# Performance work log

Hardware: AMD Instinct MI355X
Metric: run time of the kernel (lower is better)

## Reference

```python
import jax, jax.numpy as jnp
import numpy as np

N_NODES = 50000
N_EDGES = 1600000
IN_FEATS = 256
OUT_FEATS = 64


def setup_inputs() -> dict:
    key = jax.random.key(0)
    k1, k2, k3, k4, k5, k6 = jax.random.split(key, 6)
    feature = jax.random.normal(k1, (N_NODES, IN_FEATS), dtype=jnp.float32)
    src = jax.random.randint(k2, (N_EDGES,), 0, N_NODES, dtype=jnp.int32)
    dst = jax.random.randint(k3, (N_EDGES,), 0, N_NODES, dtype=jnp.int32)
    # parameters (xavier-ish scaling)
    W = jax.random.normal(k4, (OUT_FEATS, IN_FEATS), dtype=jnp.float32) * np.sqrt(2.0 / (IN_FEATS + OUT_FEATS))
    att_w = jax.random.normal(k5, (1, 2 * OUT_FEATS), dtype=jnp.float32) * np.sqrt(2.0 / (2 * OUT_FEATS + 1))
    bias = jax.random.normal(k6, (1, OUT_FEATS), dtype=jnp.float32) * np.sqrt(2.0 / (1 + OUT_FEATS))
    return {"feature": feature, "W": W, "att_w": att_w, "bias": bias, "src": src, "dst": dst}


def reference(feature, W, att_w, bias, src, dst):
    # Wh = linear(feature)   [N, out]
    Wh = feature @ W.T
    # concat([Wh_src, Wh_dst]) @ att_w.T  ==  Wh_src@a_src + Wh_dst@a_dst
    a_src = att_w[0, :OUT_FEATS]
    a_dst = att_w[0, OUT_FEATS:]
    el = Wh @ a_src  # [N]
    er = Wh @ a_dst  # [N]
    e = el[src] + er[dst]  # [E]
    e = jax.nn.leaky_relu(e, negative_slope=0.2)
    # segment softmax over incoming edges of each dst node
    e_max = jax.ops.segment_max(e, dst, num_segments=N_NODES)  # -inf for empty
    e_max = jnp.where(jnp.isfinite(e_max), e_max, 0.0)
    e_exp = jnp.exp(e - e_max[dst])
    denom = jax.ops.segment_sum(e_exp, dst, num_segments=N_NODES)
    alpha = e_exp / jnp.where(denom[dst] > 0, denom[dst], 1.0)  # [E]
    # scatter-weighted sum of source features
    h_new = jax.ops.segment_sum(alpha[:, None] * Wh[src], dst, num_segments=N_NODES)
    # residual + bias + activation
    h_new = h_new + Wh
    h_new = jax.nn.elu(h_new + bias)
    return h_new
```

## Files before the change

kernel.cpp:

```cpp
#include <hip/hip_runtime.h>
#include <hip/hip_bf16.h>
#include <math.h>

#define N_NODES 50000
#define N_EDGES 1600000
#define IN_F 256
#define OUT_F 64

#define NBUCKETS 196
#define CAP 10240
#define GEMM_BLOCKS 782
#define BK_BLOCKS 391
#define EPB 4096

typedef short short8 __attribute__((ext_vector_type(8)));
typedef float f32x4 __attribute__((ext_vector_type(4)));

__device__ __forceinline__ unsigned short f2bf(float f) {
    union { __hip_bfloat16 h; unsigned short u; } v;
    v.h = __float2bfloat16(f);
    return v.u;
}
__device__ __forceinline__ float bf2f(unsigned u) {
    return __uint_as_float(u << 16);
}

__global__ __launch_bounds__(256) void k_prep(const float* __restrict__ W,
                                              unsigned short* __restrict__ wfrag,
                                              int* __restrict__ cnt) {
    const int tid = threadIdx.x;
    if (blockIdx.x == 0 && tid < NBUCKETS) cnt[tid] = 0;
    int c = blockIdx.x * 256 + tid;
    int ct = c >> 9, kt = (c >> 6) & 7, cl = c & 63;
    int col = ct * 16 + (cl & 15);
    int kb = kt * 32 + 8 * (cl >> 4);
    const float* p = W + col * 256 + kb;
    float4 x = *(const float4*)p;
    float4 y = *(const float4*)(p + 4);
    short8 v;
    v[0] = f2bf(x.x); v[1] = f2bf(x.y); v[2] = f2bf(x.z); v[3] = f2bf(x.w);
    v[4] = f2bf(y.x); v[5] = f2bf(y.y); v[6] = f2bf(y.z); v[7] = f2bf(y.w);
    *(short8*)(wfrag + c * 8) = v;
}

__global__ __launch_bounds__(256) void k_main(const float* __restrict__ feat,
                                              const unsigned short* __restrict__ wfrag,
                                              const float* __restrict__ att_w,
                                              unsigned short* __restrict__ whb,
                                              float* __restrict__ el,
                                              float* __restrict__ er,
                                              const int* __restrict__ src,
                                              const int* __restrict__ dst,
                                              int* __restrict__ cnt,
                                              unsigned* __restrict__ pairs) {
    const int tid = threadIdx.x;

    if (blockIdx.x >= GEMM_BLOCKS) {
        __shared__ int lhist[NBUCKETS];
        __shared__ int lcur[NBUCKETS];
        const int beg = (blockIdx.x - GEMM_BLOCKS) * EPB;
        int end = beg + EPB; if (end > N_EDGES) end = N_EDGES;
        if (tid < NBUCKETS) lhist[tid] = 0;
        __syncthreads();
        for (int i = beg + tid; i < end; i += 256)
            atomicAdd(&lhist[dst[i] >> 8], 1);
        __syncthreads();
        if (tid < NBUCKETS) {
            int c = lhist[tid];
            lcur[tid] = c ? (tid * CAP + atomicAdd(&cnt[tid], c)) : 0;
        }
        __syncthreads();
        for (int i = beg + tid; i < end; i += 256) {
            int d = dst[i];
            int pos = atomicAdd(&lcur[d >> 8], 1);
            pairs[pos] = (unsigned)src[i] | ((unsigned)(d & 255) << 16);
        }
        return;
    }

    const int l = tid & 63, w = tid >> 6;
    const int l15 = l & 15, lg = l >> 4;
    const int wbase = blockIdx.x * 64 + w * 16;
    int ar = wbase + l15; if (ar > N_NODES - 1) ar = N_NODES - 1;
    const float* fbase = feat + (size_t)ar * IN_F + 8 * lg;
    const unsigned short* wfl = wfrag + l * 8;

    f32x4 acc[4];
    #pragma unroll
    for (int ct = 0; ct < 4; ++ct) acc[ct] = (f32x4){0.f, 0.f, 0.f, 0.f};

    float4 fa = *(const float4*)(fbase);
    float4 fb = *(const float4*)(fbase + 4);
    #pragma unroll
    for (int kt = 0; kt < 8; ++kt) {
        float4 na, nb;
        if (kt < 7) {
            na = *(const float4*)(fbase + (kt + 1) * 32);
            nb = *(const float4*)(fbase + (kt + 1) * 32 + 4);
        }
        short8 bf0 = *(const short8*)(wfl + (0 * 8 + kt) * 512);
        short8 bf1 = *(const short8*)(wfl + (1 * 8 + kt) * 512);
        short8 bf2 = *(const short8*)(wfl + (2 * 8 + kt) * 512);
        short8 bf3 = *(const short8*)(wfl + (3 * 8 + kt) * 512);
        short8 af;
        af[0] = f2bf(fa.x); af[1] = f2bf(fa.y); af[2] = f2bf(fa.z); af[3] = f2bf(fa.w);
        af[4] = f2bf(fb.x); af[5] = f2bf(fb.y); af[6] = f2bf(fb.z); af[7] = f2bf(fb.w);
        acc[0] = __builtin_amdgcn_mfma_f32_16x16x32_bf16(af, bf0, acc[0], 0, 0, 0);
        acc[1] = __builtin_amdgcn_mfma_f32_16x16x32_bf16(af, bf1, acc[1], 0, 0, 0);
        acc[2] = __builtin_amdgcn_mfma_f32_16x16x32_bf16(af, bf2, acc[2], 0, 0, 0);
        acc[3] = __builtin_amdgcn_mfma_f32_16x16x32_bf16(af, bf3, acc[3], 0, 0, 0);
        fa = na; fb = nb;
    }

    float asrc[4], adst[4];
    #pragma unroll
    for (int ct = 0; ct < 4; ++ct) {
        asrc[ct] = att_w[ct * 16 + l15];
        adst[ct] = att_w[64 + ct * 16 + l15];
    }
    #pragma unroll
    for (int j = 0; j < 4; ++j) {
        int row = wbase + lg * 4 + j;
        float vs = 0.f, vd = 0.f;
        #pragma unroll
        for (int ct = 0; ct < 4; ++ct) {
            float v = acc[ct][j];
            vs += v * asrc[ct];
            vd += v * adst[ct];
            if (row < N_NODES) whb[(size_t)row * OUT_F + ct * 16 + l15] = f2bf(v);
        }
        vs += __shfl_xor(vs, 1); vd += __shfl_xor(vd, 1);
        vs += __shfl_xor(vs, 2); vd += __shfl_xor(vd, 2);
        vs += __shfl_xor(vs, 4); vd += __shfl_xor(vd, 4);
        vs += __shfl_xor(vs, 8); vd += __shfl_xor(vd, 8);
        if (l15 == 0 && row < N_NODES) { el[row] = vs; er[row] = vd; }
    }
}

__global__ __launch_bounds__(1024) void k_build(const int* __restrict__ cnt,
                                                const unsigned* __restrict__ pairs,
                                                const float* __restrict__ el,
                                                const float* __restrict__ er,
                                                int* __restrict__ offs,
                                                int* __restrict__ oend,
                                                unsigned* __restrict__ csr) {
    __shared__ int lcnt[256], ssc[256], lcur[256];
    __shared__ float ler[256];
    const int b = blockIdx.x;
    const int t = threadIdx.x;
    const int ebeg = b * CAP;
    const int nE = cnt[b];

    if (t < 256) {
        lcnt[t] = 0;
        int node = b * 256 + t;
        ler[t] = (node < N_NODES) ? er[node] : 0.f;
    }
    __syncthreads();
    for (int i = t; i < nE; i += 1024)
        atomicAdd(&lcnt[(pairs[ebeg + i] >> 16) & 255], 1);
    __syncthreads();
    if (t < 256) ssc[t] = (lcnt[t] + 3) & ~3;
    __syncthreads();
    for (int d = 1; d < 256; d <<= 1) {
        int v = 0;
        if (t < 256 && t >= d) v = ssc[t - d];
        __syncthreads();
        if (t < 256) ssc[t] += v;
        __syncthreads();
    }
    if (t < 256) {
        int pc = (lcnt[t] + 3) & ~3;
        int base = ssc[t] - pc;
        lcur[t] = base;
        int node = b * 256 + t;
        if (node < N_NODES) { offs[node] = ebeg + base; oend[node] = ebeg + base + pc; }
        for (int k = lcnt[t]; k < pc; ++k) csr[ebeg + base + k] = 0;
    }
    __syncthreads();
    for (int i = t; i < nE; i += 1024) {
        unsigned v = pairs[ebeg + i];
        int n8 = (v >> 16) & 255;
        int s = v & 0xFFFFu;
        float e = el[s] + ler[n8];
        e = (e > 0.f) ? e : 0.2f * e;
        float p = __expf(e);
        int pos = atomicAdd(&lcur[n8], 1);
        csr[ebeg + pos] = (unsigned)s | ((unsigned)f2bf(p) << 16);
    }
}

__global__ __launch_bounds__(256) void k_aggr(const int* __restrict__ offs,
                                              const int* __restrict__ oend,
                                              const unsigned* __restrict__ csr,
                                              const unsigned short* __restrict__ whb,
                                              const float* __restrict__ bias,
                                              float* __restrict__ out) {
    const int wid = __builtin_amdgcn_readfirstlane(threadIdx.x >> 6);
    const int node = blockIdx.x * 4 + wid;
    const int lane = threadIdx.x & 63;
    const int fg = lane & 15, es = lane >> 4;
    const int beg = offs[node], end = oend[node];

    float acc0 = 0.f, acc1 = 0.f, acc2 = 0.f, acc3 = 0.f, den = 0.f;
    #pragma unroll 2
    for (int j = beg; j < end; j += 4) {
        unsigned e = csr[j + es];
        float p = __uint_as_float(e & 0xFFFF0000u);
        const unsigned short* wp = whb + (size_t)(e & 0xFFFFu) * OUT_F + fg * 4;
        ushort4 wv = *(const ushort4*)wp;
        den += p;
        acc0 = fmaf(p, bf2f((unsigned)wv.x), acc0);
        acc1 = fmaf(p, bf2f((unsigned)wv.y), acc1);
        acc2 = fmaf(p, bf2f((unsigned)wv.z), acc2);
        acc3 = fmaf(p, bf2f((unsigned)wv.w), acc3);
    }
    acc0 += __shfl_xor(acc0, 16); acc0 += __shfl_xor(acc0, 32);
    acc1 += __shfl_xor(acc1, 16); acc1 += __shfl_xor(acc1, 32);
    acc2 += __shfl_xor(acc2, 16); acc2 += __shfl_xor(acc2, 32);
    acc3 += __shfl_xor(acc3, 16); acc3 += __shfl_xor(acc3, 32);
    den  += __shfl_xor(den, 16);  den  += __shfl_xor(den, 32);

    if (es == 0) {
        float inv = (end > beg) ? 1.f / den : 0.f;
        ushort4 wn = *(const ushort4*)(whb + (size_t)node * OUT_F + fg * 4);
        float4 b4 = *(const float4*)(bias + fg * 4);
        float h0 = acc0 * inv + bf2f((unsigned)wn.x) + b4.x;
        float h1 = acc1 * inv + bf2f((unsigned)wn.y) + b4.y;
        float h2 = acc2 * inv + bf2f((unsigned)wn.z) + b4.z;
        float h3 = acc3 * inv + bf2f((unsigned)wn.w) + b4.w;
        h0 = (h0 > 0.f) ? h0 : __expf(h0) - 1.f;
        h1 = (h1 > 0.f) ? h1 : __expf(h1) - 1.f;
        h2 = (h2 > 0.f) ? h2 : __expf(h2) - 1.f;
        h3 = (h3 > 0.f) ? h3 : __expf(h3) - 1.f;
        *(float4*)(out + (size_t)node * OUT_F + fg * 4) = make_float4(h0, h1, h2, h3);
    }
}

extern "C" void kernel_launch(void* const* d_in, const int* in_sizes, int n_in,
                              void* d_out, int out_size, void* d_ws, size_t ws_size,
                              hipStream_t stream) {
    const float* feat  = (const float*)d_in[0];
    const float* W     = (const float*)d_in[1];
    const float* att_w = (const float*)d_in[2];
    const float* bias  = (const float*)d_in[3];
    const int*   src   = (const int*)d_in[4];
    const int*   dst   = (const int*)d_in[5];
    float* out = (float*)d_out;

    unsigned short* whb = (unsigned short*)d_ws;
    unsigned short* wfrag = whb + 3200000;
    float* el      = (float*)d_ws + 1600000 + 8192;
    float* er      = el + 50048;
    int*   offs    = (int*)(er + 50048);
    int*   oend    = offs + 50048;
    int*   cnt     = oend + 50048;
    unsigned* pairs = (unsigned*)(cnt + 512);
    unsigned* csr   = pairs + NBUCKETS * CAP;

    k_prep<<<8, 256, 0, stream>>>(W, wfrag, cnt);
    k_main<<<GEMM_BLOCKS + BK_BLOCKS, 256, 0, stream>>>(feat, wfrag, att_w, whb, el, er,
                                                        src, dst, cnt, pairs);
    k_build<<<NBUCKETS, 1024, 0, stream>>>(cnt, pairs, el, er, offs, oend, csr);
    k_aggr<<<N_NODES / 4, 256, 0, stream>>>(offs, oend, csr, whb, bias, out);
}
```

Baseline: 91.87 us.

## Stage weight fragments in LDS, preload features, vectorize edge bucketing

GEMM blocks now issue all feature loads up front and copy the bf16 weight fragments into a 32KB shared buffer once per block, so MFMA operands come from LDS rather than repeated global loads. Bucketing blocks read src/dst with int4 vector loads into registers, pack the bucket id into the top byte, and reuse those registers for both the histogram and scatter passes instead of reading dst twice. The 32KB static LDS allocation now applies to every block and may lower occupancy, and preloading 16 float4 per thread raises register pressure.

```diff
diff --git a/kernel.cpp b/kernel.cpp
--- a/kernel.cpp
+++ b/kernel.cpp
@@ -53,27 +53,57 @@
                                               const int* __restrict__ dst,
                                               int* __restrict__ cnt,
                                               unsigned* __restrict__ pairs) {
+    __shared__ unsigned short wlds[16384];
     const int tid = threadIdx.x;
 
     if (blockIdx.x >= GEMM_BLOCKS) {
-        __shared__ int lhist[NBUCKETS];
-        __shared__ int lcur[NBUCKETS];
-        const int beg = (blockIdx.x - GEMM_BLOCKS) * EPB;
-        int end = beg + EPB; if (end > N_EDGES) end = N_EDGES;
-        if (tid < NBUCKETS) lhist[tid] = 0;
-        __syncthreads();
-        for (int i = beg + tid; i < end; i += 256)
-            atomicAdd(&lhist[dst[i] >> 8], 1);
-        __syncthreads();
-        if (tid < NBUCKETS) {
-            int c = lhist[tid];
-            lcur[tid] = c ? (tid * CAP + atomicAdd(&cnt[tid], c)) : 0;
-        }
-        __syncthreads();
-        for (int i = beg + tid; i < end; i += 256) {
-            int d = dst[i];
-            int pos = atomicAdd(&lcur[d >> 8], 1);
-            pairs[pos] = (unsigned)src[i] | ((unsigned)(d & 255) << 16);
+        int* lhist = (int*)wlds;
+        int* lcur  = lhist + 256;
+        const int bbeg = (blockIdx.x - GEMM_BLOCKS) * EPB;
+
+        unsigned wreg[16];
+        #pragma unroll
+        for (int j = 0; j < 4; ++j) {
+            int e0 = bbeg + j * 1024 + tid * 4;
+            if (e0 + 3 < N_EDGES) {
+                int4 dv = *(const int4*)(dst + e0);
+                int4 sv = *(const int4*)(src + e0);
+                wreg[j*4+0] = (unsigned)sv.x | ((unsigned)(dv.x & 255) << 16) | ((unsigned)(dv.x >> 8) << 24);
+                wreg[j*4+1] = (unsigned)sv.y | ((unsigned)(dv.y & 255) << 16) | ((unsigned)(dv.y >> 8) << 24);
+                wreg[j*4+2] = (unsigned)sv.z | ((unsigned)(dv.z & 255) << 16) | ((unsigned)(dv.z >> 8) << 24);
+                wreg[j*4+3] = (unsigned)sv.w | ((unsigned)(dv.w & 255) << 16) | ((unsigned)(dv.w >> 8) << 24);
+            } else {
+                #pragma unroll
+                for (int k = 0; k < 4; ++k) {
+                    int e = e0 + k;
+                    if (e < N_EDGES) {
+                        int d = dst[e];
+                        wreg[j*4+k] = (unsigned)src[e] | ((unsigned)(d & 255) << 16) | ((unsigned)(d >> 8) << 24);
+                    } else wreg[j*4+k] = 0xFF000000u;
+                }
+            }
+        }
+        for (int i = tid; i < NBUCKETS; i += 256) lhist[i] = 0;
+        __syncthreads();
+        #pragma unroll
+        for (int k = 0; k < 16; ++k) {
+            unsigned b = wreg[k] >> 24;
+            if (b < NBUCKETS) atomicAdd(&lhist[b], 1);
+        }
+        __syncthreads();
+        for (int i = tid; i < NBUCKETS; i += 256) {
+            int c = lhist[i];
+            lcur[i] = c ? (i * CAP + atomicAdd(&cnt[i], c)) : 0;
+        }
+        __syncthreads();
+        #pragma unroll
+        for (int k = 0; k < 16; ++k) {
+            unsigned wv = wreg[k];
+            unsigned b = wv >> 24;
+            if (b < NBUCKETS) {
+                int pos = atomicAdd(&lcur[b], 1);
+                pairs[pos] = wv & 0x00FFFFFFu;
+            }
         }
         return;
     }
@@ -83,33 +113,38 @@
     const int wbase = blockIdx.x * 64 + w * 16;
     int ar = wbase + l15; if (ar > N_NODES - 1) ar = N_NODES - 1;
     const float* fbase = feat + (size_t)ar * IN_F + 8 * lg;
-    const unsigned short* wfl = wfrag + l * 8;
+
+    float4 f[16];
+    #pragma unroll
+    for (int kt = 0; kt < 8; ++kt) {
+        f[2*kt]   = *(const float4*)(fbase + kt * 32);
+        f[2*kt+1] = *(const float4*)(fbase + kt * 32 + 4);
+    }
+    #pragma unroll
+    for (int i = 0; i < 8; ++i) {
+        int c = tid + 256 * i;
+        *(short8*)(&wlds[c * 8]) = *(const short8*)(wfrag + c * 8);
+    }
+    __syncthreads();
 
     f32x4 acc[4];
     #pragma unroll
     for (int ct = 0; ct < 4; ++ct) acc[ct] = (f32x4){0.f, 0.f, 0.f, 0.f};
 
-    float4 fa = *(const float4*)(fbase);
-    float4 fb = *(const float4*)(fbase + 4);
     #pragma unroll
     for (int kt = 0; kt < 8; ++kt) {
-        float4 na, nb;
-        if (kt < 7) {
-            na = *(const float4*)(fbase + (kt + 1) * 32);
-            nb = *(const float4*)(fbase + (kt + 1) * 32 + 4);
-        }
-        short8 bf0 = *(const short8*)(wfl + (0 * 8 + kt) * 512);
-        short8 bf1 = *(const short8*)(wfl + (1 * 8 + kt) * 512);
-        short8 bf2 = *(const short8*)(wfl + (2 * 8 + kt) * 512);
-        short8 bf3 = *(const short8*)(wfl + (3 * 8 + kt) * 512);
+        float4 fa = f[2*kt], fb = f[2*kt+1];
         short8 af;
         af[0] = f2bf(fa.x); af[1] = f2bf(fa.y); af[2] = f2bf(fa.z); af[3] = f2bf(fa.w);
         af[4] = f2bf(fb.x); af[5] = f2bf(fb.y); af[6] = f2bf(fb.z); af[7] = f2bf(fb.w);
-        acc[0] = __builtin_amdgcn_mfma_f32_16x16x32_bf16(af, bf0, acc[0], 0, 0, 0);
-        acc[1] = __builtin_amdgcn_mfma_f32_16x16x32_bf16(af, bf1, acc[1], 0, 0, 0);
-        acc[2] = __builtin_amdgcn_mfma_f32_16x16x32_bf16(af, bf2, acc[2], 0, 0, 0);
-        acc[3] = __builtin_amdgcn_mfma_f32_16x16x32_bf16(af, bf3, acc[3], 0, 0, 0);
-        fa = na; fb = nb;
+        short8 b0 = *(const short8*)(&wlds[((0 * 8 + kt) * 64 + l) * 8]);
+        short8 b1 = *(const short8*)(&wlds[((1 * 8 + kt) * 64 + l) * 8]);
+        short8 b2 = *(const short8*)(&wlds[((2 * 8 + kt) * 64 + l) * 8]);
+        short8 b3 = *(const short8*)(&wlds[((3 * 8 + kt) * 64 + l) * 8]);
+        acc[0] = __builtin_amdgcn_mfma_f32_16x16x32_bf16(af, b0, acc[0], 0, 0, 0);
+        acc[1] = __builtin_amdgcn_mfma_f32_16x16x32_bf16(af, b1, acc[1], 0, 0, 0);
+        acc[2] = __builtin_amdgcn_mfma_f32_16x16x32_bf16(af, b2, acc[2], 0, 0, 0);
+        acc[3] = __builtin_amdgcn_mfma_f32_16x16x32_bf16(af, b3, acc[3], 0, 0, 0);
     }
 
     float asrc[4], adst[4];
```

New measurement: 87.15 us. -5.1%, faster.
